# Optimization experiments

Measured on AMD Instinct MI355X. Metric: run time of the kernel, lower is better.

The kernel has to match this reference:

```python
import jax, jax.numpy as jnp
import numpy as np
from jax.scipy.special import logsumexp

B0, K, T, A = 128, 8, 1024, 5
N_KCS, N_PROBLEMS = 50, 1000
MAX_LEN = K * T          # 8192 trials per student timeline
S = B0 * K               # 1024 subsequences
EPS = 1e-12


def setup_inputs() -> dict:
    rng = np.random.default_rng(0)
    lens = rng.integers(T - 128, T + 1, size=S)          # valid length per subsequence
    t = np.arange(T)
    valid = t[None, :] < lens[:, None]                   # (S,T) padding mask
    s = np.arange(S)
    # subsequence s covers slice (s%K)*T..+T of student s//K's timeline
    trial = (s // K)[:, None] * MAX_LEN + (s % K)[:, None] * T + t[None, :]
    trial = np.where(valid, trial, -1).astype(np.int32)
    problem = np.where(valid, rng.integers(0, N_PROBLEMS, (S, T)), 0).astype(np.int32)
    correct = np.where(valid, rng.integers(0, 2, (S, T)), 0).astype(np.int32)
    kc = rng.integers(0, N_KCS, S).astype(np.int32)
    ytrue_flat = -np.ones(B0 * MAX_LEN, dtype=np.int32)
    ytrue_flat[trial[valid]] = correct[valid]
    ytrue = ytrue_flat.reshape(B0, MAX_LEN)
    k1, k2, k3 = jax.random.split(jax.random.key(0), 3)
    return {
        'dynamics_logits': jax.random.normal(k1, (N_KCS, 3), dtype=jnp.float32),
        'obs_logits_kc': jax.random.normal(k2, (N_KCS, 2), dtype=jnp.float32),
        'obs_logits_problem': 0.1 * jax.random.normal(k3, (N_PROBLEMS, 2), dtype=jnp.float32),
        'ability_levels': jnp.array([-2.0, -1.0, 0.0, 1.0, 2.0], dtype=jnp.float32),
        'padded_trial_id': jnp.asarray(trial),
        'padded_problem': jnp.asarray(problem),
        'padded_correct': jnp.asarray(correct),
        'kc': jnp.asarray(kc),
        'ytrue': jnp.asarray(ytrue),
    }


def _bkt_filter(corr, dyn, pG, pS):
    """BKT HMM forward filter. corr:(B,T) int, dyn:(B,3), pG/pS:(B,T).
    Returns log predictive prob (B,T,2) of [incorrect, correct] before each trial."""
    pL = jax.nn.sigmoid(dyn[:, 0])   # p(learn)
    pF = jax.nn.sigmoid(dyn[:, 1])   # p(forget)
    pI = jax.nn.sigmoid(dyn[:, 2])   # p(known initially)
    alpha0 = jnp.stack([1.0 - pI, pI], axis=1)  # (B,2): [not-known, known]

    def step(alpha, xs):
        g, sl, y = xs                 # (B,) each
        pc0, pc1 = g, 1.0 - sl        # p(correct | state)
        p_corr = alpha[:, 0] * pc0 + alpha[:, 1] * pc1
        pred = jnp.stack([1.0 - p_corr, p_corr], axis=1)
        lik = jnp.where(y[:, None] == 1,
                        jnp.stack([pc0, pc1], axis=1),
                        jnp.stack([1.0 - pc0, 1.0 - pc1], axis=1))
        post = alpha * lik
        post = post / jnp.clip(post.sum(axis=1, keepdims=True), EPS)
        nxt = jnp.stack([post[:, 0] * (1 - pL) + post[:, 1] * pF,
                         post[:, 0] * pL + post[:, 1] * (1 - pF)], axis=1)
        return nxt, pred

    _, preds = jax.lax.scan(step, alpha0, (pG.T, pS.T, corr.T))  # preds: (T,B,2)
    return jnp.log(jnp.clip(jnp.transpose(preds, (1, 0, 2)), EPS))


def reference(dynamics_logits, obs_logits_kc, obs_logits_problem, ability_levels,
              padded_trial_id, padded_problem, padded_correct, kc, ytrue):
    b0, max_len = ytrue.shape
    a = ability_levels.shape[0]
    s_sub, t_len = padded_correct.shape
    # tile subsequence batch across ability levels (A*S rows)
    ability = jnp.repeat(ability_levels, s_sub)
    abil_ix = jnp.repeat(jnp.arange(a), s_sub)
    corr = jnp.tile(padded_correct, (a, 1))
    prob = jnp.tile(padded_problem, (a, 1))
    kc_t = jnp.tile(kc, (a,))
    tid = jnp.tile(padded_trial_id, (a, 1))

    dyn = dynamics_logits[kc_t]                                       # (AS,3)
    obs = obs_logits_kc[kc_t][:, None, :] + obs_logits_problem[prob]  # (AS,T,2)
    pG = jax.nn.sigmoid(obs[..., 0] + ability[:, None])  # p(correct | not known)
    pS = jax.nn.sigmoid(obs[..., 1] - ability[:, None])  # p(incorrect | known)
    logprob_pred = _bkt_filter(corr, dyn, pG, pS)        # (AS,T,2)

    # scatter back into per-ability flat student timelines
    adj = tid + abil_ix[:, None] * (b0 * max_len)
    adj = jnp.where(tid == -1, -1, adj).reshape(-1)
    n_flat = a * b0 * max_len
    idx = jnp.where(adj > -1, adj, n_flat)               # out-of-range -> dropped
    buf = jnp.zeros((n_flat, 2), dtype=logprob_pred.dtype)
    buf = buf.at[idx].set(logprob_pred.reshape(-1, 2), mode='drop')
    result = jnp.transpose(buf.reshape(a, b0, max_len, 2), (1, 0, 2, 3))  # (B0,A,L,2)

    # sequential Bayesian averaging over ability levels (uniform prior)
    mask = ytrue > -1
    yc = jnp.where(mask, ytrue, 0)
    obs_ll = jnp.take_along_axis(result, yc[:, None, :, None].astype(jnp.int32), axis=3)[..., 0]
    obs_ll = obs_ll * mask[:, None, :]
    prefix = jnp.cumsum(obs_ll, axis=2) - obs_ll          # exclusive cumsum over time
    logw = prefix - logsumexp(prefix, axis=1, keepdims=True)
    logpred = logsumexp(result + logw[..., None], axis=1)  # (B0,L,2)
    return logpred
```

## Files before the change

### kernel.cpp

```cpp
#include <hip/hip_runtime.h>
#include <hip/hip_fp16.h>
#include <math.h>

#define A 5
#define S 1024
#define T 1024
#define KCH 8
#define B0 128
#define L 8192
#define NPROB 1000
#define EPSF 1e-12f
#define CHUNK 8
#define PPB 2

__device__ __forceinline__ float sigmoidf_(float x) {
    return 1.0f / (1.0f + __expf(-x));
}

union H2U { unsigned u; __half2 h; };

__global__ __launch_bounds__(256) void bkt_filter_kernel(
    const float* __restrict__ dyn_logits,
    const float* __restrict__ obs_kc,
    const float* __restrict__ obs_prob,
    const float* __restrict__ abil,
    const int*   __restrict__ trial,
    const int*   __restrict__ problem,
    const int*   __restrict__ correct,
    const int*   __restrict__ kc,
    __half2* __restrict__ result,
    float* __restrict__ pfloc,
    float* __restrict__ sumchunk)
{
    __shared__ float2 s_e[NPROB];
    __shared__ float  s_m0[PPB][4];
    __shared__ float  s_llw[PPB];

    for (int i = threadIdx.x; i < NPROB; i += 256) {
        float2 op = ((const float2*)obs_prob)[i];
        s_e[i] = make_float2(__expf(-op.x), __expf(op.y));
    }
    __syncthreads();

    int wv = threadIdx.x >> 6;
    int lane = threadIdx.x & 63;
    int pib = wv >> 1;
    int half = wv & 1;
    int pair = blockIdx.x * PPB + pib;
    int a = pair >> 10;
    int s = pair & (S - 1);

    float ability = abil[a];
    int kcs = kc[s];
    float pL = sigmoidf_(dyn_logits[kcs * 3 + 0]);
    float pF = sigmoidf_(dyn_logits[kcs * 3 + 1]);
    float pI = sigmoidf_(dyn_logits[kcs * 3 + 2]);
    float ok0 = obs_kc[kcs * 2 + 0];
    float ok1 = obs_kc[kcs * 2 + 1];
    float t00 = 1.0f - pL, t01 = pF, t10 = pL, t11 = 1.0f - pF;
    float c0 = __expf(-ok0 - ability);
    float c1 = __expf( ok1 - ability);

    int t0 = half * (T / 2) + lane * CHUNK;
    const int4* pv4 = (const int4*)(problem + (size_t)s * T + t0);
    const int4* cv4 = (const int4*)(correct + (size_t)s * T + t0);
    const int4* tv4 = (const int4*)(trial   + (size_t)s * T + t0);
    int4 pva = pv4[0], pvb = pv4[1];
    int4 cva = cv4[0], cvb = cv4[1];
    int4 tva = tv4[0], tvb = tv4[1];

    int pj[8] = {pva.x, pva.y, pva.z, pva.w, pvb.x, pvb.y, pvb.z, pvb.w};
    int cj[8] = {cva.x, cva.y, cva.z, cva.w, cvb.x, cvb.y, cvb.z, cvb.w};
    int vj[8] = {tva.x, tva.y, tva.z, tva.w, tvb.x, tvb.y, tvb.z, tvb.w};
    int cmask = 0, vmask = 0;
    #pragma unroll
    for (int j = 0; j < 8; ++j) {
        cmask |= (cj[j] & 1) << j;
        vmask |= (vj[j] != -1) << j;
    }

    float pc0a[8], pc1a[8];
    float p00 = 1.0f, p01 = 0.0f, p10 = 0.0f, p11 = 1.0f;
    #pragma unroll
    for (int j = 0; j < 8; ++j) {
        float2 e = s_e[pj[j]];
        float pc0 = __builtin_amdgcn_rcpf(1.0f + e.x * c0);
        float pc1 = __builtin_amdgcn_rcpf(1.0f + e.y * c1);
        pc0a[j] = pc0; pc1a[j] = pc1;
        bool c = (cmask >> j) & 1;
        float lik0 = c ? pc0 : 1.0f - pc0;
        float lik1 = c ? pc1 : 1.0f - pc1;
        float r0 = lik0 * p00, r1 = lik1 * p10;
        float r2 = lik0 * p01, r3 = lik1 * p11;
        p00 = t00 * r0 + t01 * r1;
        p10 = t10 * r0 + t11 * r1;
        p01 = t00 * r2 + t01 * r3;
        p11 = t10 * r2 + t11 * r3;
        if ((j & 3) == 3) {
            float inv = __builtin_amdgcn_rcpf(p00 + p01 + p10 + p11);
            p00 *= inv; p01 *= inv; p10 *= inv; p11 *= inv;
        }
    }

    float q00 = p00, q01 = p01, q10 = p10, q11 = p11;
    #pragma unroll
    for (int off = 1; off < 64; off <<= 1) {
        float o00 = __shfl_up(q00, off);
        float o01 = __shfl_up(q01, off);
        float o10 = __shfl_up(q10, off);
        float o11 = __shfl_up(q11, off);
        if (lane >= off) {
            float n00 = q00 * o00 + q01 * o10;
            float n01 = q00 * o01 + q01 * o11;
            float n10 = q10 * o00 + q11 * o10;
            float n11 = q10 * o01 + q11 * o11;
            float inv = __builtin_amdgcn_rcpf(n00 + n01 + n10 + n11);
            q00 = n00 * inv; q01 = n01 * inv; q10 = n10 * inv; q11 = n11 * inv;
        }
    }
    if (half == 0 && lane == 63) {
        s_m0[pib][0] = q00; s_m0[pib][1] = q01;
        s_m0[pib][2] = q10; s_m0[pib][3] = q11;
    }
    __syncthreads();

    float e00 = __shfl_up(q00, 1), e01 = __shfl_up(q01, 1);
    float e10 = __shfl_up(q10, 1), e11 = __shfl_up(q11, 1);
    if (lane == 0) { e00 = 1.0f; e01 = 0.0f; e10 = 0.0f; e11 = 1.0f; }
    if (half == 1) {
        float m00 = s_m0[pib][0], m01 = s_m0[pib][1];
        float m10 = s_m0[pib][2], m11 = s_m0[pib][3];
        float n00 = e00 * m00 + e01 * m10;
        float n01 = e00 * m01 + e01 * m11;
        float n10 = e10 * m00 + e11 * m10;
        float n11 = e10 * m01 + e11 * m11;
        e00 = n00; e01 = n01; e10 = n10; e11 = n11;
    }
    float a0 = e00 * (1.0f - pI) + e01 * pI;
    float a1 = e10 * (1.0f - pI) + e11 * pI;
    {
        float inv = __builtin_amdgcn_rcpf(fmaxf(a0 + a1, EPSF));
        a0 *= inv; a1 *= inv;
    }

    float ll[8];
    float llsum = 0.0f;
    #pragma unroll
    for (int j = 0; j < 8; ++j) {
        float pc0 = pc0a[j], pc1 = pc1a[j];
        bool c = (cmask >> j) & 1;
        bool valid = (vmask >> j) & 1;
        float p_corr = a0 * pc0 + a1 * pc1;
        float p1v = p_corr, p0v = 1.0f - p_corr;
        float py = c ? p1v : p0v;
        float llj = valid ? __logf(fmaxf(py, EPSF)) : 0.0f;
        ll[j] = llj; llsum += llj;
        pc0a[j] = valid ? p0v : 1.0f;
        pc1a[j] = valid ? p1v : 1.0f;
        float lik0 = c ? pc0 : 1.0f - pc0;
        float lik1 = c ? pc1 : 1.0f - pc1;
        float qq0 = a0 * lik0, qq1 = a1 * lik1;
        float invq = __builtin_amdgcn_rcpf(fmaxf(qq0 + qq1, EPSF));
        qq0 *= invq; qq1 *= invq;
        a0 = qq0 * t00 + qq1 * t01;
        a1 = qq0 * t10 + qq1 * t11;
    }

    float incl = llsum;
    #pragma unroll
    for (int off = 1; off < 64; off <<= 1) {
        float o = __shfl_up(incl, off);
        if (lane >= off) incl += o;
    }
    float excl = incl - llsum;
    if (half == 0 && lane == 63) s_llw[pib] = incl;
    __syncthreads();
    int b = s >> 3, chunk = s & 7;
    if (half == 1) {
        float w0 = s_llw[pib];
        excl += w0;
        if (lane == 63)
            sumchunk[((size_t)a * B0 + b) * KCH + chunk] = w0 + incl;
    }

    unsigned ru[8];
    #pragma unroll
    for (int j = 0; j < 8; ++j) {
        H2U cv_;
        cv_.h = __floats2half2_rn(pc0a[j], pc1a[j]);
        ru[j] = cv_.u;
    }
    __half2* res_row = result + ((size_t)pair * T + t0);
    ((uint4*)res_row)[0] = make_uint4(ru[0], ru[1], ru[2], ru[3]);
    ((uint4*)res_row)[1] = make_uint4(ru[4], ru[5], ru[6], ru[7]);

    float* pf_row = pfloc + ((size_t)pair * T + t0);
    float run = excl;
    float pw[8];
    #pragma unroll
    for (int j = 0; j < 8; ++j) { pw[j] = run; run += ll[j]; }
    ((float4*)pf_row)[0] = make_float4(pw[0], pw[1], pw[2], pw[3]);
    ((float4*)pf_row)[1] = make_float4(pw[4], pw[5], pw[6], pw[7]);
}

__global__ __launch_bounds__(256) void combine_kernel(
    const float* __restrict__ pfloc,
    const __half2* __restrict__ result,
    const float* __restrict__ sumchunk,
    float* __restrict__ out)
{
    int s_sub = blockIdx.x;
    int b = s_sub >> 3, chunk = s_sub & 7;
    int t0 = threadIdx.x * 4;

    float pf[A][4];
    float2 pp[A][4];
    #pragma unroll
    for (int a = 0; a < A; ++a) {
        float base = 0.0f;
        for (int k = 0; k < chunk; ++k)
            base += sumchunk[((size_t)a * B0 + b) * KCH + k];
        size_t off = ((size_t)a * S + s_sub) * T + t0;
        float4 f = *(const float4*)(pfloc + off);
        pf[a][0] = f.x + base; pf[a][1] = f.y + base;
        pf[a][2] = f.z + base; pf[a][3] = f.w + base;
        uint4 q = *(const uint4*)(result + off);
        unsigned uu[4] = {q.x, q.y, q.z, q.w};
        #pragma unroll
        for (int j = 0; j < 4; ++j) {
            H2U cv_; cv_.u = uu[j];
            pp[a][j] = __half22float2(cv_.h);
        }
    }

    float o[8];
    #pragma unroll
    for (int j = 0; j < 4; ++j) {
        float pm = -INFINITY;
        #pragma unroll
        for (int a = 0; a < A; ++a) pm = fmaxf(pm, pf[a][j]);
        float Se = 0.0f, S0 = 0.0f, S1 = 0.0f;
        #pragma unroll
        for (int a = 0; a < A; ++a) {
            float e = __expf(pf[a][j] - pm);
            Se += e;
            S0 += e * pp[a][j].x;
            S1 += e * pp[a][j].y;
        }
        float ls = __logf(Se);
        o[2*j]   = __logf(S0) - ls;
        o[2*j+1] = __logf(S1) - ls;
    }
    float* op = out + 2 * ((size_t)b * L + chunk * T + t0);
    ((float4*)op)[0] = make_float4(o[0], o[1], o[2], o[3]);
    ((float4*)op)[1] = make_float4(o[4], o[5], o[6], o[7]);
}

extern "C" void kernel_launch(void* const* d_in, const int* in_sizes, int n_in,
                              void* d_out, int out_size, void* d_ws, size_t ws_size,
                              hipStream_t stream) {
    const float* dyn  = (const float*)d_in[0];
    const float* okc  = (const float*)d_in[1];
    const float* oprb = (const float*)d_in[2];
    const float* ab   = (const float*)d_in[3];
    const int* trial  = (const int*)d_in[4];
    const int* prob   = (const int*)d_in[5];
    const int* corr   = (const int*)d_in[6];
    const int* kc     = (const int*)d_in[7];
    float* out = (float*)d_out;

    __half2* result = (__half2*)d_ws;
    float* pfloc = (float*)((char*)d_ws + (size_t)A * S * T * 4);
    float* sumchunk = pfloc + (size_t)A * S * T;

    bkt_filter_kernel<<<(A * S) / PPB, 256, 0, stream>>>(
        dyn, okc, oprb, ab, trial, prob, corr, kc, result, pfloc, sumchunk);
    combine_kernel<<<B0 * KCH, 256, 0, stream>>>(pfloc, result, sumchunk, out);
}
```

Baseline: 39.41 us.

## Precompute lengths and exp table in prep kernel, cut normalizations, vectorize chunk sums

After: 41.65 us. 5.7% more time.

```diff
diff --git a/kernel.cpp b/kernel.cpp
--- a/kernel.cpp
+++ b/kernel.cpp
@@ -19,15 +19,39 @@
 
 union H2U { unsigned u; __half2 h; };
 
+__global__ __launch_bounds__(256) void prep_kernel(
+    const int* __restrict__ trial,
+    const float* __restrict__ obs_prob,
+    int* __restrict__ lens,
+    float2* __restrict__ etab)
+{
+    if (blockIdx.x == 256) {
+        for (int i = threadIdx.x; i < NPROB; i += 256) {
+            float2 op = ((const float2*)obs_prob)[i];
+            etab[i] = make_float2(__expf(-op.x), __expf(op.y));
+        }
+        return;
+    }
+    int wv = threadIdx.x >> 6, lane = threadIdx.x & 63;
+    int s = blockIdx.x * 4 + wv;
+    const int* row = trial + (size_t)s * T + 896;
+    int v1 = row[lane] != -1;
+    int v2 = row[64 + lane] != -1;
+    unsigned long long m1 = __ballot(v1);
+    unsigned long long m2 = __ballot(v2);
+    if (lane == 0)
+        lens[s] = 896 + __popcll(m1) + __popcll(m2);
+}
+
 __global__ __launch_bounds__(256) void bkt_filter_kernel(
     const float* __restrict__ dyn_logits,
     const float* __restrict__ obs_kc,
-    const float* __restrict__ obs_prob,
     const float* __restrict__ abil,
-    const int*   __restrict__ trial,
     const int*   __restrict__ problem,
     const int*   __restrict__ correct,
     const int*   __restrict__ kc,
+    const int*   __restrict__ lens,
+    const float2* __restrict__ etab,
     __half2* __restrict__ result,
     float* __restrict__ pfloc,
     float* __restrict__ sumchunk)
@@ -36,10 +60,8 @@
     __shared__ float  s_m0[PPB][4];
     __shared__ float  s_llw[PPB];
 
-    for (int i = threadIdx.x; i < NPROB; i += 256) {
-        float2 op = ((const float2*)obs_prob)[i];
-        s_e[i] = make_float2(__expf(-op.x), __expf(op.y));
-    }
+    for (int i = threadIdx.x; i < NPROB; i += 256)
+        s_e[i] = etab[i];
     __syncthreads();
 
     int wv = threadIdx.x >> 6;
@@ -52,6 +74,7 @@
 
     float ability = abil[a];
     int kcs = kc[s];
+    int len_s = lens[s];
     float pL = sigmoidf_(dyn_logits[kcs * 3 + 0]);
     float pF = sigmoidf_(dyn_logits[kcs * 3 + 1]);
     float pI = sigmoidf_(dyn_logits[kcs * 3 + 2]);
@@ -64,19 +87,16 @@
     int t0 = half * (T / 2) + lane * CHUNK;
     const int4* pv4 = (const int4*)(problem + (size_t)s * T + t0);
     const int4* cv4 = (const int4*)(correct + (size_t)s * T + t0);
-    const int4* tv4 = (const int4*)(trial   + (size_t)s * T + t0);
     int4 pva = pv4[0], pvb = pv4[1];
     int4 cva = cv4[0], cvb = cv4[1];
-    int4 tva = tv4[0], tvb = tv4[1];
 
     int pj[8] = {pva.x, pva.y, pva.z, pva.w, pvb.x, pvb.y, pvb.z, pvb.w};
     int cj[8] = {cva.x, cva.y, cva.z, cva.w, cvb.x, cvb.y, cvb.z, cvb.w};
-    int vj[8] = {tva.x, tva.y, tva.z, tva.w, tvb.x, tvb.y, tvb.z, tvb.w};
     int cmask = 0, vmask = 0;
     #pragma unroll
     for (int j = 0; j < 8; ++j) {
         cmask |= (cj[j] & 1) << j;
-        vmask |= (vj[j] != -1) << j;
+        vmask |= ((t0 + j) < len_s) << j;
     }
 
     float pc0a[8], pc1a[8];
@@ -114,19 +134,23 @@
             float n01 = q00 * o01 + q01 * o11;
             float n10 = q10 * o00 + q11 * o10;
             float n11 = q10 * o01 + q11 * o11;
-            float inv = __builtin_amdgcn_rcpf(n00 + n01 + n10 + n11);
-            q00 = n00 * inv; q01 = n01 * inv; q10 = n10 * inv; q11 = n11 * inv;
+            q00 = n00; q01 = n01; q10 = n10; q11 = n11;
         }
     }
     if (half == 0 && lane == 63) {
-        s_m0[pib][0] = q00; s_m0[pib][1] = q01;
-        s_m0[pib][2] = q10; s_m0[pib][3] = q11;
+        float inv = __builtin_amdgcn_rcpf(fmaxf(q00 + q01 + q10 + q11, 1e-30f));
+        s_m0[pib][0] = q00 * inv; s_m0[pib][1] = q01 * inv;
+        s_m0[pib][2] = q10 * inv; s_m0[pib][3] = q11 * inv;
     }
     __syncthreads();
 
     float e00 = __shfl_up(q00, 1), e01 = __shfl_up(q01, 1);
     float e10 = __shfl_up(q10, 1), e11 = __shfl_up(q11, 1);
     if (lane == 0) { e00 = 1.0f; e01 = 0.0f; e10 = 0.0f; e11 = 1.0f; }
+    {
+        float inv = __builtin_amdgcn_rcpf(fmaxf(e00 + e01 + e10 + e11, 1e-30f));
+        e00 *= inv; e01 *= inv; e10 *= inv; e11 *= inv;
+    }
     if (half == 1) {
         float m00 = s_m0[pib][0], m01 = s_m0[pib][1];
         float m10 = s_m0[pib][2], m11 = s_m0[pib][3];
@@ -150,20 +174,25 @@
         float pc0 = pc0a[j], pc1 = pc1a[j];
         bool c = (cmask >> j) & 1;
         bool valid = (vmask >> j) & 1;
-        float p_corr = a0 * pc0 + a1 * pc1;
-        float p1v = p_corr, p0v = 1.0f - p_corr;
-        float py = c ? p1v : p0v;
+        float num = a0 * pc0 + a1 * pc1;
+        float den = a0 + a1;
+        float rden = __builtin_amdgcn_rcpf(den);
+        float pcor = num * rden;
+        float p0v = 1.0f - pcor;
+        float py = c ? pcor : p0v;
         float llj = valid ? __logf(fmaxf(py, EPSF)) : 0.0f;
         ll[j] = llj; llsum += llj;
         pc0a[j] = valid ? p0v : 1.0f;
-        pc1a[j] = valid ? p1v : 1.0f;
+        pc1a[j] = valid ? pcor : 1.0f;
         float lik0 = c ? pc0 : 1.0f - pc0;
         float lik1 = c ? pc1 : 1.0f - pc1;
-        float qq0 = a0 * lik0, qq1 = a1 * lik1;
-        float invq = __builtin_amdgcn_rcpf(fmaxf(qq0 + qq1, EPSF));
-        qq0 *= invq; qq1 *= invq;
-        a0 = qq0 * t00 + qq1 * t01;
-        a1 = qq0 * t10 + qq1 * t11;
+        float q0 = a0 * lik0, q1 = a1 * lik1;
+        a0 = q0 * t00 + q1 * t01;
+        a1 = q0 * t10 + q1 * t11;
+        if ((j & 3) == 3) {
+            float inv = __builtin_amdgcn_rcpf(fmaxf(a0 + a1, EPSF));
+            a0 *= inv; a1 *= inv;
+        }
     }
 
     float incl = llsum;
@@ -217,9 +246,13 @@
     float2 pp[A][4];
     #pragma unroll
     for (int a = 0; a < A; ++a) {
+        const float* scp = sumchunk + ((size_t)a * B0 + b) * KCH;
+        float4 ca = ((const float4*)scp)[0];
+        float4 cb = ((const float4*)scp)[1];
+        float cs[8] = {ca.x, ca.y, ca.z, ca.w, cb.x, cb.y, cb.z, cb.w};
         float base = 0.0f;
-        for (int k = 0; k < chunk; ++k)
-            base += sumchunk[((size_t)a * B0 + b) * KCH + k];
+        #pragma unroll
+        for (int k = 0; k < 8; ++k) base += (k < chunk) ? cs[k] : 0.0f;
         size_t off = ((size_t)a * S + s_sub) * T + t0;
         float4 f = *(const float4*)(pfloc + off);
         pf[a][0] = f.x + base; pf[a][1] = f.y + base;
@@ -269,11 +302,15 @@
     const int* kc     = (const int*)d_in[7];
     float* out = (float*)d_out;
 
-    __half2* result = (__half2*)d_ws;
-    float* pfloc = (float*)((char*)d_ws + (size_t)A * S * T * 4);
-    float* sumchunk = pfloc + (size_t)A * S * T;
-
+    char* wsp = (char*)d_ws;
+    __half2* result = (__half2*)wsp;
+    float* pfloc    = (float*)(wsp + (size_t)A * S * T * 4);
+    float* sumchunk = (float*)(wsp + (size_t)A * S * T * 8);
+    int* lens       = (int*)(wsp + (size_t)A * S * T * 8 + 20480);
+    float2* etab    = (float2*)(wsp + (size_t)A * S * T * 8 + 20480 + 4096);
+
+    prep_kernel<<<257, 256, 0, stream>>>(trial, oprb, lens, etab);
     bkt_filter_kernel<<<(A * S) / PPB, 256, 0, stream>>>(
-        dyn, okc, oprb, ab, trial, prob, corr, kc, result, pfloc, sumchunk);
+        dyn, okc, ab, prob, corr, kc, lens, etab, result, pfloc, sumchunk);
     combine_kernel<<<B0 * KCH, 256, 0, stream>>>(pfloc, result, sumchunk, out);
 }
```
